# Kernel tuning notes

Hardware: AMD Instinct MI355X
Metric: run time of the kernel (lower is better)

Reference implementation:

```python
import jax, jax.numpy as jnp
import numpy as np

NEG_SLOPE = 0.1

def mlp(x, w1, b1, w2, b2):
    # MLP(sizes): Linear -> LeakyReLU(0.1) -> Linear
    return jax.nn.leaky_relu(x @ w1 + b1, NEG_SLOPE) @ w2 + b2

def _seg_mean(vals, idx, n):
    s = jax.ops.segment_sum(vals, idx, num_segments=n)
    cnt = jax.ops.segment_sum(jnp.ones((vals.shape[0],), vals.dtype), idx, num_segments=n)
    return s / jnp.maximum(cnt, 1.0)[:, None]

def setup_inputs() -> dict:
    key = jax.random.key(0)
    ks = iter(jax.random.split(key, 40))
    N, F, H, E = 100000, 64, 128, 800000
    Ha = H // 2  # hidden_dim/2 = 64
    def lin(k, i, o):
        k1, k2 = jax.random.split(k)
        return (jax.random.normal(k1, (i, o), jnp.float32) * (1.0 / np.sqrt(i)),
                jax.random.normal(k2, (o,), jnp.float32) * 0.01)
    inp = {}
    inp['feat'] = jax.random.normal(next(ks), (N, F), jnp.float32)
    inp['pi_feat'] = jax.random.normal(next(ks), (N, 4), jnp.float32)
    inp['level'] = jax.random.uniform(next(ks), (N, 1), jnp.float32)
    inp['bit_position'] = jax.random.uniform(next(ks), (E, 1), jnp.float32)
    inp['is_po'] = jax.random.randint(next(ks), (N,), 0, 2, jnp.int32)
    inp['is_module'] = jax.random.randint(next(ks), (N,), 0, 2, jnp.int32)
    inp['src_m'] = jax.random.randint(next(ks), (E,), 0, N, jnp.int32)
    inp['dst_m'] = jax.random.randint(next(ks), (E,), 0, N, jnp.int32)
    inp['src_g'] = jax.random.randint(next(ks), (E,), 0, N, jnp.int32)
    inp['dst_g'] = jax.random.randint(next(ks), (E,), 0, N, jnp.int32)
    # mlp_pi: 4 -> H/2 -> H
    inp['pi_w1'], inp['pi_b1'] = lin(next(ks), 4, Ha)
    inp['pi_w2'], inp['pi_b2'] = lin(next(ks), Ha, H)
    # mlp_neigh_module: H + F + 1 -> H/2 -> H
    inp['nm_w1'], inp['nm_b1'] = lin(next(ks), H + F + 1, Ha)
    inp['nm_w2'], inp['nm_b2'] = lin(next(ks), Ha, H)
    # mlp_neigh_gate: H + F -> H/2 -> H
    inp['ng_w1'], inp['ng_b1'] = lin(next(ks), H + F, Ha)
    inp['ng_w2'], inp['ng_b2'] = lin(next(ks), Ha, H)
    # mlp_global: 1 -> H/2 -> H
    inp['g_w1'], inp['g_b1'] = lin(next(ks), 1, Ha)
    inp['g_w2'], inp['g_b2'] = lin(next(ks), Ha, H)
    # mlp_out: 2H -> H -> 1
    inp['o_w1'], inp['o_b1'] = lin(next(ks), 2 * H, H)
    inp['o_w2'], inp['o_b2'] = lin(next(ks), H, 1)
    return inp

def reference(feat, pi_feat, level, bit_position,
              pi_w1, pi_b1, pi_w2, pi_b2,
              nm_w1, nm_b1, nm_w2, nm_b2,
              ng_w1, ng_b1, ng_w2, ng_b2,
              g_w1, g_b1, g_w2, g_b2,
              o_w1, o_b1, o_w2, o_b2,
              is_po, is_module, src_m, dst_m, src_g, dst_g):
    N = feat.shape[0]
    # PI init embedding (mlp_pi)
    h0 = mlp(pi_feat, pi_w1, pi_b1, pi_w2, pi_b2)            # [N, H]
    # module-edge message passing: m = src h, pos = bit_position; mean reduce
    m = h0[src_m]                                            # [E, H] irregular gather
    neigh_m = _seg_mean(m, dst_m, N)                         # [N, H]
    pos_m = _seg_mean(bit_position, dst_m, N)                # [N, 1]
    # nodes_func_module, agg_choice==0: cat(neigh, pos, feat) -> mlp_neigh_module
    h_m = mlp(jnp.concatenate([neigh_m, pos_m, feat], axis=1), nm_w1, nm_b1, nm_w2, nm_b2)
    # gate-edge message passing
    neigh_g = _seg_mean(h0[src_g], dst_g, N)                 # [N, H]
    h_g = mlp(jnp.concatenate([neigh_g, feat], axis=1), ng_w1, ng_b1, ng_w2, ng_b2)
    # ReLU on non-PO nodes only
    keep = (is_po != 1)[:, None]
    h_m = jnp.where(keep, jax.nn.relu(h_m), h_m)
    h_g = jnp.where(keep, jax.nn.relu(h_g), h_g)
    # per-node-type update (hetero apply_nodes)
    h = jnp.where((is_module == 1)[:, None], h_m, h_g)       # [N, H]
    # global branch + readout
    hg = mlp(level, g_w1, g_b1, g_w2, g_b2)                  # [N, H]
    out = mlp(jnp.concatenate([h, hg], axis=1), o_w1, o_b1, o_w2, o_b2)  # [N, 1]
    return out
```

## Files before the change

### kernel.cpp

```cpp
#include <hip/hip_runtime.h>

typedef __bf16 bf16x8 __attribute__((ext_vector_type(8)));
typedef float f32x4 __attribute__((ext_vector_type(4)));
typedef unsigned short u16;
typedef unsigned int u32;
typedef unsigned long long u64;

__device__ __forceinline__ u16 f2b(float f) {
  return __builtin_bit_cast(u16, (__bf16)f);
}
__device__ __forceinline__ float b2f_lo(u32 pk) {
  return __builtin_bit_cast(float, pk << 16);
}
__device__ __forceinline__ float b2f_hi(u32 pk) {
  return __builtin_bit_cast(float, pk & 0xffff0000u);
}
__device__ __forceinline__ float leaky(float x) { return x > 0.f ? x : 0.1f * x; }
__device__ __forceinline__ f32x4 mfma16(bf16x8 a, bf16x8 b, f32x4 c) {
  return __builtin_amdgcn_mfma_f32_16x16x32_bf16(a, b, c, 0, 0, 0);
}

#define P64 72
#define P128 136
#define CAP 16
#define RSTRIDE 32

#define SBLK 256
#define PBLK 256

__global__ __launch_bounds__(256) void k_zero(int* rec, int* spillcnt, int N) {
  int n = blockIdx.x * 256 + threadIdx.x;
  if (n < N) {
    rec[(size_t)n * RSTRIDE] = 0;
    rec[(size_t)n * RSTRIDE + 1] = 0;
  }
  if (n == 0) *spillcnt = 0;
}

__global__ __launch_bounds__(256) void k_prep(
    const float* nm_w1, const float* ng_w1, const float* nm_w2, const float* ng_w2,
    const float* o_w1, const float* o_b1, const float* g_w2, const float* g_b2,
    const float* pi_w2, const float* pi_b2, const int* is_module,
    u16* wt_yc, float* bias_y, u16* wt_f1m, u16* wt_f1g, float* w_pos,
    u16* wt2m, u16* wt2g, u16* wt_oh, u16* gt, float* bp, u32* mbits, int N) {
  int i = blockIdx.x * 256 + threadIdx.x;
  if (i < 9216) {
    int ty = i / 4608, rem = i % 4608, n = rem / P64, k = rem % P64;
    float v = 0.f;
    if (k < 64) {
      const float* w1 = ty ? ng_w1 : nm_w1;
      for (int t = 0; t < 128; t++) v += pi_w2[k * 128 + t] * w1[t * 64 + n];
    }
    wt_yc[i] = f2b(v);
    return;
  }
  i -= 9216;
  if (i < 128) {
    int ty = i >> 6, n = i & 63;
    const float* w1 = ty ? ng_w1 : nm_w1;
    float v = 0.f;
    for (int t = 0; t < 128; t++) v += pi_b2[t] * w1[t * 64 + n];
    bias_y[i] = v;
    return;
  }
  i -= 128;
  if (i < 4608) {
    int n = i / P64, k = i % P64;
    wt_f1m[i] = f2b(k < 64 ? nm_w1[(129 + k) * 64 + n] : 0.f);
    return;
  }
  i -= 4608;
  if (i < 4608) {
    int n = i / P64, k = i % P64;
    wt_f1g[i] = f2b(k < 64 ? ng_w1[(128 + k) * 64 + n] : 0.f);
    return;
  }
  i -= 4608;
  if (i < 64) { w_pos[i] = nm_w1[128 * 64 + i]; return; }
  i -= 64;
  if (i < 9216) {
    int n = i / P64, k = i % P64;
    wt2m[i] = f2b(k < 64 ? nm_w2[k * 128 + n] : 0.f);
    return;
  }
  i -= 9216;
  if (i < 9216) {
    int n = i / P64, k = i % P64;
    wt2g[i] = f2b(k < 64 ? ng_w2[k * 128 + n] : 0.f);
    return;
  }
  i -= 9216;
  if (i < 17408) {
    int n = i / P128, k = i % P128;
    wt_oh[i] = f2b(k < 128 ? o_w1[k * 128 + n] : 0.f);
    return;
  }
  i -= 17408;
  if (i < 9216) {
    int n = i / P64, k = i % P64;
    float v = 0.f;
    if (k < 64)
      for (int t = 0; t < 128; t++) v += g_w2[k * 128 + t] * o_w1[(128 + t) * 128 + n];
    gt[i] = f2b(v);
    return;
  }
  i -= 9216;
  if (i < 128) {
    float s = o_b1[i];
    for (int t = 0; t < 128; t++) s += g_b2[t] * o_w1[(128 + t) * 128 + i];
    bp[i] = s;
    return;
  }
  i -= 128;
  {
    int n = i;
    int lane = threadIdx.x & 63;
    bool v = (n < N) && (is_module[n] == 1);
    u64 b = __ballot(v);
    if (lane == 0 && n < N) mbits[n >> 5] = (u32)b;
    if (lane == 32 && n < N) mbits[n >> 5] = (u32)(b >> 32);
  }
}

__global__ __launch_bounds__(512) void k_mid(
    const int* src_m, const int* dst_m, const int* src_g, const int* dst_g,
    const u32* mbits, const float* bitpos, int* rec, u64* spill, int* spillcnt,
    int E,
    const float* pf, const float* feat, const float* pi_w1, const float* pi_b1,
    const u16* wt_yc_g, const float* bias_y, const u16* wt_f1m_g, const u16* wt_f1g_g,
    const float* nm_b1, const float* ng_b1, u16* y0, u16* f1, int N) {
  __shared__ __align__(16) u16 wyc[2][64 * P64];
  __shared__ __align__(16) u16 wf[2][64 * P64];
  __shared__ __align__(16) u16 tbuf[8][16 * P64];

  if (blockIdx.x < SBLK) {
    int tid = blockIdx.x * 512 + threadIdx.x;
    const int STR = SBLK * 512;
    for (int v0 = tid; v0 < E; v0 += STR * 4) {
      int dd[8], ss[8];
      float bb[8];
      bool el[8];
#pragma unroll
      for (int k = 0; k < 4; k++) {
        int vt = v0 + k * STR;
        bool vv = vt < E;
#pragma unroll
        for (int j = 0; j < 2; j++) {
          int x = k * 2 + j;
          el[x] = false;
          dd[x] = 0; ss[x] = 0; bb[x] = 0.f;
          if (vv) {
            int e = vt * 2 + j;
            int d = (e < E) ? dst_m[e] : dst_g[e - E];
            dd[x] = d;
            bool bit = (mbits[d >> 5] >> (d & 31)) & 1;
            el[x] = (e < E) ? bit : !bit;
            if (el[x]) {
              if (e < E) { ss[x] = src_m[e]; bb[x] = bitpos[e]; }
              else ss[x] = src_g[e - E];
            }
          }
        }
      }
      int cc[8];
#pragma unroll
      for (int x = 0; x < 8; x++)
        if (el[x]) cc[x] = atomicAdd(&rec[(size_t)dd[x] * RSTRIDE], 1);
#pragma unroll
      for (int x = 0; x < 8; x++) {
        if (!el[x]) continue;
        int vt = v0 + (x >> 1) * STR;
        int e = vt * 2 + (x & 1);
        int d = dd[x], s = ss[x], c = cc[x];
        if (e < E) {
          if (c < CAP) {
            int bp12 = (int)(bb[x] * 4096.f);
            if (bp12 > 4095) bp12 = 4095;
            rec[(size_t)d * RSTRIDE + 2 + c] = (s << 12) | bp12;
          } else {
            int p = atomicAdd(spillcnt, 1);
            spill[p] = ((u64)(u32)d << 32) | (u32)s;
            atomicAdd((float*)&rec[(size_t)d * RSTRIDE + 1], bb[x]);
          }
        } else {
          if (c < CAP) {
            rec[(size_t)d * RSTRIDE + 2 + c] = s << 12;
          } else {
            int p = atomicAdd(spillcnt, 1);
            spill[p] = ((u64)(u32)d << 32) | (u32)s;
          }
        }
      }
    }
    return;
  }

  int pb = blockIdx.x - SBLK;
  for (int i = threadIdx.x; i < 2304; i += 512) {
    ((u32*)wyc[0])[i] = ((const u32*)wt_yc_g)[i];
    ((u32*)wyc[1])[i] = ((const u32*)wt_yc_g)[2304 + i];
    ((u32*)wf[0])[i] = ((const u32*)wt_f1m_g)[i];
    ((u32*)wf[1])[i] = ((const u32*)wt_f1g_g)[i];
  }

  int lane = threadIdx.x & 63, wv = threadIdx.x >> 6;
  int lid = lane & 15, q = lane >> 4;

  bf16x8 w1f[4];
#pragma unroll
  for (int nt = 0; nt < 4; nt++) {
    bf16x8 f;
#pragma unroll
    for (int j = 0; j < 8; j++) {
      int k = q * 8 + j;
      f[j] = (__bf16)((k < 4) ? pi_w1[k * 64 + nt * 16 + lid] : 0.f);
    }
    w1f[nt] = f;
  }
  __syncthreads();

  int nbat = (N + 15) >> 4;
  for (int b0 = pb * 8; b0 < nbat; b0 += PBLK * 8) {
    int b = b0 + wv;
    int batch = b < nbat ? b : nbat - 1;
    int id = batch * 16 + lid;
    if (id >= N) id = N - 1;

    bf16x8 a;
#pragma unroll
    for (int j = 0; j < 8; j++)
      a[j] = (__bf16)((q == 0 && j < 4) ? pf[(size_t)id * 4 + j] : 0.f);
    f32x4 z1[4];
#pragma unroll
    for (int nt = 0; nt < 4; nt++) {
      f32x4 c = {0.f, 0.f, 0.f, 0.f};
      z1[nt] = mfma16(a, w1f[nt], c);
    }
    __syncthreads();
#pragma unroll
    for (int nt = 0; nt < 4; nt++) {
      float bb = pi_b1[nt * 16 + lid];
#pragma unroll
      for (int r = 0; r < 4; r++)
        tbuf[wv][(q * 4 + r) * P64 + nt * 16 + lid] = f2b(leaky(z1[nt][r] + bb));
    }
    __syncthreads();
    bf16x8 a20 = *(const bf16x8*)&tbuf[wv][lid * P64 + q * 8];
    bf16x8 a21 = *(const bf16x8*)&tbuf[wv][lid * P64 + 32 + q * 8];

    int idr_[4];
#pragma unroll
    for (int r = 0; r < 4; r++) {
      int ii = batch * 16 + q * 4 + r;
      idr_[r] = ii < N ? ii : N - 1;
    }

#pragma unroll
    for (int ty = 0; ty < 2; ty++) {
#pragma unroll
      for (int nt = 0; nt < 4; nt++) {
        f32x4 c = {0.f, 0.f, 0.f, 0.f};
        c = mfma16(a20, *(const bf16x8*)&wyc[ty][(nt * 16 + lid) * P64 + q * 8], c);
        c = mfma16(a21, *(const bf16x8*)&wyc[ty][(nt * 16 + lid) * P64 + 32 + q * 8], c);
        float by = bias_y[ty * 64 + nt * 16 + lid];
#pragma unroll
        for (int r = 0; r < 4; r++)
          y0[(size_t)idr_[r] * 128 + ty * 64 + nt * 16 + lid] = f2b(c[r] + by);
      }
    }

    bf16x8 af[2];
#pragma unroll
    for (int kt = 0; kt < 2; kt++) {
      const float4* p = (const float4*)(feat + (size_t)id * 64 + kt * 32 + q * 8);
      float4 xa = p[0], xb = p[1];
      bf16x8 f;
      f[0] = (__bf16)xa.x; f[1] = (__bf16)xa.y; f[2] = (__bf16)xa.z; f[3] = (__bf16)xa.w;
      f[4] = (__bf16)xb.x; f[5] = (__bf16)xb.y; f[6] = (__bf16)xb.z; f[7] = (__bf16)xb.w;
      af[kt] = f;
    }
#pragma unroll
    for (int nt = 0; nt < 4; nt++) {
      f32x4 cm = {0.f, 0.f, 0.f, 0.f}, cg = {0.f, 0.f, 0.f, 0.f};
#pragma unroll
      for (int kt = 0; kt < 2; kt++) {
        cm = mfma16(af[kt], *(const bf16x8*)&wf[0][(nt * 16 + lid) * P64 + kt * 32 + q * 8], cm);
        cg = mfma16(af[kt], *(const bf16x8*)&wf[1][(nt * 16 + lid) * P64 + kt * 32 + q * 8], cg);
      }
      float bm = nm_b1[nt * 16 + lid], bg = ng_b1[nt * 16 + lid];
#pragma unroll
      for (int r = 0; r < 4; r++) {
        int idr = idr_[r];
        bool mod = (mbits[idr >> 5] >> (idr & 31)) & 1;
        f1[(size_t)idr * 64 + nt * 16 + lid] = f2b(mod ? cm[r] + bm : cg[r] + bg);
      }
    }
  }
}

__global__ __launch_bounds__(256) void k_gather(const u16* y0, const int* rec,
                                                const u64* spill, const int* spillcnt,
                                                const u32* mbits, const u16* f1,
                                                const float* w_pos, u16* z1a, int N) {
  int n = (blockIdx.x * 256 + threadIdx.x) >> 6;
  int lane = threadIdx.x & 63;
  if (n >= N) return;
  bool mod = (mbits[n >> 5] >> (n & 31)) & 1;
  int sub = lane >> 5, l32 = lane & 31;
  int rv = (lane < 18) ? rec[(size_t)n * RSTRIDE + lane] : 0;
  int cnt = __shfl(rv, 0);
  float pspill = __builtin_bit_cast(float, __shfl(rv, 1));
  int inl = cnt < CAP ? cnt : CAP;
  float myb = 0.f;
  if (mod && lane >= 2 && lane < 18 && (lane - 2) < inl)
    myb = (float)(rv & 4095) * (1.f / 4096.f);
  const u32* yrow = (const u32*)y0;
  int halfo = mod ? 0 : 32;
  float a0 = 0.f, a1 = 0.f;
  for (int j = 0; j < inl; j += 2) {
    int e2 = j + sub;
    if (e2 < inl) {
      int s = (int)(((u32)__shfl(rv, 2 + e2)) >> 12);
      u32 pk = yrow[(size_t)s * 64 + halfo + l32];
      a0 += b2f_lo(pk);
      a1 += b2f_hi(pk);
    }
  }
  if (cnt > CAP) {
    int sc = *spillcnt;
    for (int base = 0; base < sc; base += 64) {
      int i = base + lane;
      u64 ent = (i < sc) ? spill[i] : 0xffffffffffffffffull;
      bool m = ((int)(ent >> 32) == n);
      u64 bal = __ballot(m);
      int slo = (int)(ent & 0xffffffffu);
      while (bal) {
        int l = __ffsll((long long)bal) - 1;
        bal &= bal - 1;
        int s = __shfl(slo, l);
        if (sub == 0) {
          u32 pk = yrow[(size_t)s * 64 + halfo + l32];
          a0 += b2f_lo(pk);
          a1 += b2f_hi(pk);
        }
      }
    }
  }
  a0 += __shfl_xor(a0, 32);
  a1 += __shfl_xor(a1, 32);
#pragma unroll
  for (int off = 1; off < 64; off <<= 1) myb += __shfl_xor(myb, off);
  float psum = pspill + myb;
  float inv = 1.f / (float)(cnt > 1 ? cnt : 1);
  if (sub == 0) {
    u32 fp = ((const u32*)f1)[(size_t)n * 32 + l32];
    float z0 = a0 * inv + b2f_lo(fp);
    float z1v = a1 * inv + b2f_hi(fp);
    if (mod) {
      float pm = psum * inv;
      float2 wp = ((const float2*)w_pos)[l32];
      z0 += pm * wp.x;
      z1v += pm * wp.y;
    }
    ((u32*)z1a)[(size_t)n * 32 + l32] = (u32)f2b(leaky(z0)) | ((u32)f2b(leaky(z1v)) << 16);
  }
}

__global__ __launch_bounds__(512) void k_tail(const u16* z1a, const u16* wt2m_g,
                                              const u16* wt2g_g, const float* nm_b2,
                                              const float* ng_b2, const u32* mbits,
                                              const int* is_po, const float* level,
                                              const float* g_w1, const float* g_b1,
                                              const u16* wt_oh_g, const u16* gt_g,
                                              const float* bp_g, const float* o_w2,
                                              const float* o_b2, float* out, int N) {
  __shared__ __align__(16) u16 w2[2][128 * P64];
  __shared__ __align__(16) u16 wt_oh[128 * P128];
  __shared__ __align__(16) u16 gt[128 * P64];
  __shared__ __align__(16) u16 tbuf[8][16 * P128];
  for (int i = threadIdx.x; i < 128 * P64 / 2; i += 512) {
    ((u32*)w2[0])[i] = ((const u32*)wt2m_g)[i];
    ((u32*)w2[1])[i] = ((const u32*)wt2g_g)[i];
    ((u32*)gt)[i] = ((const u32*)gt_g)[i];
  }
  for (int i = threadIdx.x; i < 128 * P128 / 2; i += 512)
    ((u32*)wt_oh)[i] = ((const u32*)wt_oh_g)[i];

  int lane = threadIdx.x & 63, wv = threadIdx.x >> 6;
  int lid = lane & 15, q = lane >> 4;
  int nbat = (N + 15) >> 4;

  float gw[2][8], gb[2][8];
#pragma unroll
  for (int kt = 0; kt < 2; kt++)
#pragma unroll
    for (int j = 0; j < 8; j++) {
      int k = kt * 32 + q * 8 + j;
      gw[kt][j] = g_w1[k];
      gb[kt][j] = g_b1[k];
    }
  float w2o[8], bpv[8];
#pragma unroll
  for (int nt = 0; nt < 8; nt++) {
    w2o[nt] = o_w2[nt * 16 + lid];
    bpv[nt] = bp_g[nt * 16 + lid];
  }
  float b2m[8], b2g[8];
#pragma unroll
  for (int nt = 0; nt < 8; nt++) {
    b2m[nt] = nm_b2[nt * 16 + lid];
    b2g[nt] = ng_b2[nt * 16 + lid];
  }
  float ob2 = o_b2[0];
  __syncthreads();

  for (int b0 = blockIdx.x * 8; b0 < nbat; b0 += gridDim.x * 8) {
    int b = b0 + wv;
    int batch = b < nbat ? b : nbat - 1;
    int id = batch * 16 + lid;
    if (id >= N) id = N - 1;

    bf16x8 a0 = *(const bf16x8*)(z1a + (size_t)id * 64 + q * 8);
    bf16x8 a1 = *(const bf16x8*)(z1a + (size_t)id * 64 + 32 + q * 8);
    bool mod_[4], kp_[4];
#pragma unroll
    for (int r = 0; r < 4; r++) {
      int ii = batch * 16 + q * 4 + r;
      if (ii >= N) ii = N - 1;
      mod_[r] = (mbits[ii >> 5] >> (ii & 31)) & 1;
      kp_[r] = (is_po[ii] != 1);
    }
    __syncthreads();
#pragma unroll
    for (int nt = 0; nt < 8; nt++) {
      f32x4 cm = {0.f, 0.f, 0.f, 0.f}, cg = {0.f, 0.f, 0.f, 0.f};
      cm = mfma16(a0, *(const bf16x8*)&w2[0][(nt * 16 + lid) * P64 + q * 8], cm);
      cm = mfma16(a1, *(const bf16x8*)&w2[0][(nt * 16 + lid) * P64 + 32 + q * 8], cm);
      cg = mfma16(a0, *(const bf16x8*)&w2[1][(nt * 16 + lid) * P64 + q * 8], cg);
      cg = mfma16(a1, *(const bf16x8*)&w2[1][(nt * 16 + lid) * P64 + 32 + q * 8], cg);
#pragma unroll
      for (int r = 0; r < 4; r++) {
        float v = mod_[r] ? cm[r] + b2m[nt] : cg[r] + b2g[nt];
        if (kp_[r]) v = fmaxf(v, 0.f);
        tbuf[wv][(q * 4 + r) * P128 + nt * 16 + lid] = f2b(v);
      }
    }
    __syncthreads();

    bf16x8 ah[4];
#pragma unroll
    for (int kt = 0; kt < 4; kt++)
      ah[kt] = *(const bf16x8*)&tbuf[wv][lid * P128 + kt * 32 + q * 8];
    float lv = level[id];
    bf16x8 ag[2];
#pragma unroll
    for (int kt = 0; kt < 2; kt++)
#pragma unroll
      for (int j = 0; j < 8; j++)
        ag[kt][j] = (__bf16)leaky(lv * gw[kt][j] + gb[kt][j]);

    f32x4 accv[8];
#pragma unroll
    for (int nt = 0; nt < 8; nt++) {
      f32x4 c = {0.f, 0.f, 0.f, 0.f};
#pragma unroll
      for (int kt = 0; kt < 4; kt++)
        c = mfma16(ah[kt], *(const bf16x8*)&wt_oh[(nt * 16 + lid) * P128 + kt * 32 + q * 8], c);
#pragma unroll
      for (int kt = 0; kt < 2; kt++)
        c = mfma16(ag[kt], *(const bf16x8*)&gt[(nt * 16 + lid) * P64 + kt * 32 + q * 8], c);
      accv[nt] = c;
    }
    float p[4];
#pragma unroll
    for (int r = 0; r < 4; r++) {
      float s = 0.f;
#pragma unroll
      for (int nt = 0; nt < 8; nt++) s += leaky(accv[nt][r] + bpv[nt]) * w2o[nt];
      p[r] = s;
    }
#pragma unroll
    for (int r = 0; r < 4; r++)
#pragma unroll
      for (int off = 1; off < 16; off <<= 1) p[r] += __shfl_xor(p[r], off, 16);
    if (lid == 0) {
#pragma unroll
      for (int r = 0; r < 4; r++) {
        int idr = batch * 16 + q * 4 + r;
        if (idr >= N) idr = N - 1;
        out[idr] = p[r] + ob2;
      }
    }
  }
}

extern "C" void kernel_launch(void* const* d_in, const int* in_sizes, int n_in,
                              void* d_out, int out_size, void* d_ws, size_t ws_size,
                              hipStream_t stream) {
  const float* feat = (const float*)d_in[0];
  const float* pi_feat = (const float*)d_in[1];
  const float* level = (const float*)d_in[2];
  const float* bitpos = (const float*)d_in[3];
  const int* is_po = (const int*)d_in[4];
  const int* is_module = (const int*)d_in[5];
  const int* src_m = (const int*)d_in[6];
  const int* dst_m = (const int*)d_in[7];
  const int* src_g = (const int*)d_in[8];
  const int* dst_g = (const int*)d_in[9];
  const float* pi_w1 = (const float*)d_in[10];
  const float* pi_b1 = (const float*)d_in[11];
  const float* pi_w2 = (const float*)d_in[12];
  const float* pi_b2 = (const float*)d_in[13];
  const float* nm_w1 = (const float*)d_in[14];
  const float* nm_b1 = (const float*)d_in[15];
  const float* nm_w2 = (const float*)d_in[16];
  const float* nm_b2 = (const float*)d_in[17];
  const float* ng_w1 = (const float*)d_in[18];
  const float* ng_b1 = (const float*)d_in[19];
  const float* ng_w2 = (const float*)d_in[20];
  const float* ng_b2 = (const float*)d_in[21];
  const float* g_w1 = (const float*)d_in[22];
  const float* g_b1 = (const float*)d_in[23];
  const float* g_w2 = (const float*)d_in[24];
  const float* g_b2 = (const float*)d_in[25];
  const float* o_w1 = (const float*)d_in[26];
  const float* o_b1 = (const float*)d_in[27];
  const float* o_w2 = (const float*)d_in[28];
  const float* o_b2 = (const float*)d_in[29];

  int N = in_sizes[0] / 64;
  int E = in_sizes[3];

  char* ws = (char*)d_ws;
  size_t off = 0;
  auto alloc = [&](size_t bytes) {
    char* p = ws + off;
    off += (bytes + 255) & ~(size_t)255;
    return p;
  };
  int* rec = (int*)alloc(((size_t)N * RSTRIDE + 64) * 4);
  int* spillcnt = (int*)alloc(16);
  u64* spill = (u64*)alloc((size_t)2 * E * 8);
  u32* mbits = (u32*)alloc((size_t)((N + 31) / 32) * 4);
  u16* y0 = (u16*)alloc((size_t)N * 128 * 2);
  u16* f1 = (u16*)alloc((size_t)N * 64 * 2);
  u16* z1a = (u16*)alloc((size_t)N * 64 * 2);
  u16* wt_yc = (u16*)alloc(9216 * 2);
  float* bias_y = (float*)alloc(128 * 4);
  u16* wt_f1m = (u16*)alloc(4608 * 2);
  u16* wt_f1g = (u16*)alloc(4608 * 2);
  float* w_pos = (float*)alloc(64 * 4);
  u16* wt2m = (u16*)alloc(9216 * 2);
  u16* wt2g = (u16*)alloc(9216 * 2);
  u16* wt_oh = (u16*)alloc(17408 * 2);
  u16* gt = (u16*)alloc(9216 * 2);
  float* bp = (float*)alloc(128 * 4);

  k_zero<<<(N + 255) / 256, 256, 0, stream>>>(rec, spillcnt, N);

  int prep_items = 63808 + ((N + 63) & ~63);
  k_prep<<<(prep_items + 255) / 256, 256, 0, stream>>>(
      nm_w1, ng_w1, nm_w2, ng_w2, o_w1, o_b1, g_w2, g_b2, pi_w2, pi_b2, is_module,
      wt_yc, bias_y, wt_f1m, wt_f1g, w_pos, wt2m, wt2g, wt_oh, gt, bp, mbits, N);

  k_mid<<<SBLK + PBLK, 512, 0, stream>>>(
      src_m, dst_m, src_g, dst_g, mbits, bitpos, rec, spill, spillcnt, E,
      pi_feat, feat, pi_w1, pi_b1, wt_yc, bias_y, wt_f1m, wt_f1g,
      nm_b1, ng_b1, y0, f1, N);

  k_gather<<<(N * 64 + 255) / 256, 256, 0, stream>>>(
      y0, rec, spill, spillcnt, mbits, f1, w_pos, z1a, N);

  k_tail<<<256, 512, 0, stream>>>(z1a, wt2m, wt2g, nm_b2, ng_b2, mbits, is_po,
                                  level, g_w1, g_b1, wt_oh, gt, bp, o_w2, o_b2,
                                  (float*)d_out, N);
}
```

Before: 269.4 us.

## Fuse neighbor gather into tail kernel via per-wave LDS staging

Merges the per-node gather/mean kernel into the tail MLP kernel. Each wave now gathers its 16 nodes sequentially, writes the layer-1 activations into a per-wave LDS buffer, and feeds them straight to the MFMA stages, so the z1a round trip through global memory is gone. It also drops the block-wide __syncthreads around the per-wave tbuf, since each wave only touches its own slice. The cost is that the irregular gather now runs on only 256 blocks of 512 threads with one node at a time per wave, instead of a dense one-wave-per-node launch, which cuts memory-level parallelism for the latency-bound gather.

```diff
diff --git a/kernel.cpp b/kernel.cpp
--- a/kernel.cpp
+++ b/kernel.cpp
@@ -298,130 +298,128 @@
   }
 }
 
-__global__ __launch_bounds__(256) void k_gather(const u16* y0, const int* rec,
-                                                const u64* spill, const int* spillcnt,
-                                                const u32* mbits, const u16* f1,
-                                                const float* w_pos, u16* z1a, int N) {
-  int n = (blockIdx.x * 256 + threadIdx.x) >> 6;
-  int lane = threadIdx.x & 63;
-  if (n >= N) return;
-  bool mod = (mbits[n >> 5] >> (n & 31)) & 1;
+__global__ __launch_bounds__(512) void k_gt(
+    const u16* y0, const int* rec, const u64* spill, const int* spillcnt,
+    const u32* mbits, const u16* f1, const float* w_pos,
+    const u16* wt2m_g, const u16* wt2g_g, const float* nm_b2, const float* ng_b2,
+    const int* is_po, const float* level, const float* g_w1, const float* g_b1,
+    const u16* wt_oh_g, const u16* gt_g, const float* bp_g, const float* o_w2,
+    const float* o_b2, float* out, int N) {
+  __shared__ __align__(16) u16 w2[2][128 * P64];
+  __shared__ __align__(16) u16 wt_oh[128 * P128];
+  __shared__ __align__(16) u16 gt[128 * P64];
+  __shared__ __align__(16) u16 tbuf[8][16 * P128];
+  __shared__ __align__(16) u32 zl[8][16][36];
+  for (int i = threadIdx.x; i < 128 * P64 / 2; i += 512) {
+    ((u32*)w2[0])[i] = ((const u32*)wt2m_g)[i];
+    ((u32*)w2[1])[i] = ((const u32*)wt2g_g)[i];
+    ((u32*)gt)[i] = ((const u32*)gt_g)[i];
+  }
+  for (int i = threadIdx.x; i < 128 * P128 / 2; i += 512)
+    ((u32*)wt_oh)[i] = ((const u32*)wt_oh_g)[i];
+
+  int lane = threadIdx.x & 63, wv = threadIdx.x >> 6;
+  int lid = lane & 15, q = lane >> 4;
   int sub = lane >> 5, l32 = lane & 31;
-  int rv = (lane < 18) ? rec[(size_t)n * RSTRIDE + lane] : 0;
-  int cnt = __shfl(rv, 0);
-  float pspill = __builtin_bit_cast(float, __shfl(rv, 1));
-  int inl = cnt < CAP ? cnt : CAP;
-  float myb = 0.f;
-  if (mod && lane >= 2 && lane < 18 && (lane - 2) < inl)
-    myb = (float)(rv & 4095) * (1.f / 4096.f);
+  int nbat = (N + 15) >> 4;
+
+  float gw[2][8], gb[2][8];
+#pragma unroll
+  for (int kt = 0; kt < 2; kt++)
+#pragma unroll
+    for (int j = 0; j < 8; j++) {
+      int k = kt * 32 + q * 8 + j;
+      gw[kt][j] = g_w1[k];
+      gb[kt][j] = g_b1[k];
+    }
+  float w2o[8], bpv[8];
+#pragma unroll
+  for (int nt = 0; nt < 8; nt++) {
+    w2o[nt] = o_w2[nt * 16 + lid];
+    bpv[nt] = bp_g[nt * 16 + lid];
+  }
+  float b2m[8], b2g[8];
+#pragma unroll
+  for (int nt = 0; nt < 8; nt++) {
+    b2m[nt] = nm_b2[nt * 16 + lid];
+    b2g[nt] = ng_b2[nt * 16 + lid];
+  }
+  float ob2 = o_b2[0];
+  __syncthreads();
+
   const u32* yrow = (const u32*)y0;
-  int halfo = mod ? 0 : 32;
-  float a0 = 0.f, a1 = 0.f;
-  for (int j = 0; j < inl; j += 2) {
-    int e2 = j + sub;
-    if (e2 < inl) {
-      int s = (int)(((u32)__shfl(rv, 2 + e2)) >> 12);
-      u32 pk = yrow[(size_t)s * 64 + halfo + l32];
-      a0 += b2f_lo(pk);
-      a1 += b2f_hi(pk);
-    }
-  }
-  if (cnt > CAP) {
-    int sc = *spillcnt;
-    for (int base = 0; base < sc; base += 64) {
-      int i = base + lane;
-      u64 ent = (i < sc) ? spill[i] : 0xffffffffffffffffull;
-      bool m = ((int)(ent >> 32) == n);
-      u64 bal = __ballot(m);
-      int slo = (int)(ent & 0xffffffffu);
-      while (bal) {
-        int l = __ffsll((long long)bal) - 1;
-        bal &= bal - 1;
-        int s = __shfl(slo, l);
-        if (sub == 0) {
+
+  for (int b0 = blockIdx.x * 8; b0 < nbat; b0 += gridDim.x * 8) {
+    int b = b0 + wv;
+    int batch = b < nbat ? b : nbat - 1;
+
+    for (int nn = 0; nn < 16; nn++) {
+      int n = batch * 16 + nn;
+      if (n >= N) n = N - 1;
+      bool mod = (mbits[n >> 5] >> (n & 31)) & 1;
+      int rv = (lane < 18) ? rec[(size_t)n * RSTRIDE + lane] : 0;
+      int cnt = __shfl(rv, 0);
+      float pspill = __builtin_bit_cast(float, __shfl(rv, 1));
+      int inl = cnt < CAP ? cnt : CAP;
+      float myb = 0.f;
+      if (mod && lane >= 2 && lane < 18 && (lane - 2) < inl)
+        myb = (float)(rv & 4095) * (1.f / 4096.f);
+      int halfo = mod ? 0 : 32;
+      float a0 = 0.f, a1 = 0.f;
+      for (int j = 0; j < inl; j += 2) {
+        int e2 = j + sub;
+        if (e2 < inl) {
+          int s = (int)(((u32)__shfl(rv, 2 + e2)) >> 12);
           u32 pk = yrow[(size_t)s * 64 + halfo + l32];
           a0 += b2f_lo(pk);
           a1 += b2f_hi(pk);
         }
       }
-    }
-  }
-  a0 += __shfl_xor(a0, 32);
-  a1 += __shfl_xor(a1, 32);
-#pragma unroll
-  for (int off = 1; off < 64; off <<= 1) myb += __shfl_xor(myb, off);
-  float psum = pspill + myb;
-  float inv = 1.f / (float)(cnt > 1 ? cnt : 1);
-  if (sub == 0) {
-    u32 fp = ((const u32*)f1)[(size_t)n * 32 + l32];
-    float z0 = a0 * inv + b2f_lo(fp);
-    float z1v = a1 * inv + b2f_hi(fp);
-    if (mod) {
-      float pm = psum * inv;
-      float2 wp = ((const float2*)w_pos)[l32];
-      z0 += pm * wp.x;
-      z1v += pm * wp.y;
-    }
-    ((u32*)z1a)[(size_t)n * 32 + l32] = (u32)f2b(leaky(z0)) | ((u32)f2b(leaky(z1v)) << 16);
-  }
-}
-
-__global__ __launch_bounds__(512) void k_tail(const u16* z1a, const u16* wt2m_g,
-                                              const u16* wt2g_g, const float* nm_b2,
-                                              const float* ng_b2, const u32* mbits,
-                                              const int* is_po, const float* level,
-                                              const float* g_w1, const float* g_b1,
-                                              const u16* wt_oh_g, const u16* gt_g,
-                                              const float* bp_g, const float* o_w2,
-                                              const float* o_b2, float* out, int N) {
-  __shared__ __align__(16) u16 w2[2][128 * P64];
-  __shared__ __align__(16) u16 wt_oh[128 * P128];
-  __shared__ __align__(16) u16 gt[128 * P64];
-  __shared__ __align__(16) u16 tbuf[8][16 * P128];
-  for (int i = threadIdx.x; i < 128 * P64 / 2; i += 512) {
-    ((u32*)w2[0])[i] = ((const u32*)wt2m_g)[i];
-    ((u32*)w2[1])[i] = ((const u32*)wt2g_g)[i];
-    ((u32*)gt)[i] = ((const u32*)gt_g)[i];
-  }
-  for (int i = threadIdx.x; i < 128 * P128 / 2; i += 512)
-    ((u32*)wt_oh)[i] = ((const u32*)wt_oh_g)[i];
-
-  int lane = threadIdx.x & 63, wv = threadIdx.x >> 6;
-  int lid = lane & 15, q = lane >> 4;
-  int nbat = (N + 15) >> 4;
-
-  float gw[2][8], gb[2][8];
-#pragma unroll
-  for (int kt = 0; kt < 2; kt++)
-#pragma unroll
-    for (int j = 0; j < 8; j++) {
-      int k = kt * 32 + q * 8 + j;
-      gw[kt][j] = g_w1[k];
-      gb[kt][j] = g_b1[k];
-    }
-  float w2o[8], bpv[8];
-#pragma unroll
-  for (int nt = 0; nt < 8; nt++) {
-    w2o[nt] = o_w2[nt * 16 + lid];
-    bpv[nt] = bp_g[nt * 16 + lid];
-  }
-  float b2m[8], b2g[8];
-#pragma unroll
-  for (int nt = 0; nt < 8; nt++) {
-    b2m[nt] = nm_b2[nt * 16 + lid];
-    b2g[nt] = ng_b2[nt * 16 + lid];
-  }
-  float ob2 = o_b2[0];
-  __syncthreads();
-
-  for (int b0 = blockIdx.x * 8; b0 < nbat; b0 += gridDim.x * 8) {
-    int b = b0 + wv;
-    int batch = b < nbat ? b : nbat - 1;
+      if (cnt > CAP) {
+        int sc = *spillcnt;
+        for (int base = 0; base < sc; base += 64) {
+          int i = base + lane;
+          u64 ent = (i < sc) ? spill[i] : 0xffffffffffffffffull;
+          bool m = ((int)(ent >> 32) == n);
+          u64 bal = __ballot(m);
+          int slo = (int)(ent & 0xffffffffu);
+          while (bal) {
+            int l = __ffsll((long long)bal) - 1;
+            bal &= bal - 1;
+            int s = __shfl(slo, l);
+            if (sub == 0) {
+              u32 pk = yrow[(size_t)s * 64 + halfo + l32];
+              a0 += b2f_lo(pk);
+              a1 += b2f_hi(pk);
+            }
+          }
+        }
+      }
+      a0 += __shfl_xor(a0, 32);
+      a1 += __shfl_xor(a1, 32);
+#pragma unroll
+      for (int off = 1; off < 64; off <<= 1) myb += __shfl_xor(myb, off);
+      float psum = pspill + myb;
+      float inv = 1.f / (float)(cnt > 1 ? cnt : 1);
+      if (sub == 0) {
+        u32 fp = ((const u32*)f1)[(size_t)n * 32 + l32];
+        float z0 = a0 * inv + b2f_lo(fp);
+        float z1v = a1 * inv + b2f_hi(fp);
+        if (mod) {
+          float pm = psum * inv;
+          float2 wp = ((const float2*)w_pos)[l32];
+          z0 += pm * wp.x;
+          z1v += pm * wp.y;
+        }
+        zl[wv][nn][l32] = (u32)f2b(leaky(z0)) | ((u32)f2b(leaky(z1v)) << 16);
+      }
+    }
+
     int id = batch * 16 + lid;
     if (id >= N) id = N - 1;
-
-    bf16x8 a0 = *(const bf16x8*)(z1a + (size_t)id * 64 + q * 8);
-    bf16x8 a1 = *(const bf16x8*)(z1a + (size_t)id * 64 + 32 + q * 8);
+    const u16* zr = (const u16*)zl[wv][lid];
+    bf16x8 a0 = *(const bf16x8*)&zr[q * 8];
+    bf16x8 a1 = *(const bf16x8*)&zr[32 + q * 8];
     bool mod_[4], kp_[4];
 #pragma unroll
     for (int r = 0; r < 4; r++) {
@@ -430,7 +428,6 @@
       mod_[r] = (mbits[ii >> 5] >> (ii & 31)) & 1;
       kp_[r] = (is_po[ii] != 1);
     }
-    __syncthreads();
 #pragma unroll
     for (int nt = 0; nt < 8; nt++) {
       f32x4 cm = {0.f, 0.f, 0.f, 0.f}, cg = {0.f, 0.f, 0.f, 0.f};
@@ -445,7 +442,6 @@
         tbuf[wv][(q * 4 + r) * P128 + nt * 16 + lid] = f2b(v);
       }
     }
-    __syncthreads();
 
     bf16x8 ah[4];
 #pragma unroll
@@ -544,7 +540,6 @@
   u32* mbits = (u32*)alloc((size_t)((N + 31) / 32) * 4);
   u16* y0 = (u16*)alloc((size_t)N * 128 * 2);
   u16* f1 = (u16*)alloc((size_t)N * 64 * 2);
-  u16* z1a = (u16*)alloc((size_t)N * 64 * 2);
   u16* wt_yc = (u16*)alloc(9216 * 2);
   float* bias_y = (float*)alloc(128 * 4);
   u16* wt_f1m = (u16*)alloc(4608 * 2);
@@ -568,10 +563,8 @@
       pi_feat, feat, pi_w1, pi_b1, wt_yc, bias_y, wt_f1m, wt_f1g,
       nm_b1, ng_b1, y0, f1, N);
 
-  k_gather<<<(N * 64 + 255) / 256, 256, 0, stream>>>(
-      y0, rec, spill, spillcnt, mbits, f1, w_pos, z1a, N);
-
-  k_tail<<<256, 512, 0, stream>>>(z1a, wt2m, wt2g, nm_b2, ng_b2, mbits, is_po,
-                                  level, g_w1, g_b1, wt_oh, gt, bp, o_w2, o_b2,
-                                  (float*)d_out, N);
-}
+  k_gt<<<256, 512, 0, stream>>>(
+      y0, rec, spill, spillcnt, mbits, f1, w_pos,
+      wt2m, wt2g, nm_b2, ng_b2, is_po, level, g_w1, g_b1,
+      wt_oh, gt, bp, o_w2, o_b2, (float*)d_out, N);
+}
```

Measured after the change: 401.9 us. 49.2% more time.
